# Kernel tuning notes

Measured on AMD Instinct MI355X. Metric: run time of the kernel, lower is better.

Reference implementation:

```python
import jax, jax.numpy as jnp
import numpy as np

T, U, H, P, UC = 256, 512, 64, 1024, 10000
LAMBDA_T = 0.1      # temporal decay rate (Flashback default scale)
LAMBDA_S = 100.0    # spatial decay rate
DAY = 86400.0


def setup_inputs() -> dict:
    key = jax.random.key(0)
    ks = jax.random.split(key, 12)
    sc = 0.02
    x = jax.random.randint(ks[0], (T, U), 0, P)
    # timestamps, increasing along the sequence axis (checkin order)
    t = jnp.sort(jax.random.uniform(ks[1], (T, U)) * (7.0 * DAY), axis=0)
    t_slot = jax.random.randint(ks[2], (T, U), 0, 168)
    s = jax.random.normal(ks[3], (T, U, 2))
    y = jax.random.randint(ks[4], (T, U), 0, P)
    h = jnp.zeros((U, H), jnp.float32)
    active_user = jax.random.randint(ks[5], (U,), 0, UC)
    poi_emb = jax.random.normal(ks[6], (P, H)) * sc
    user_emb = jax.random.normal(ks[7], (UC, H)) * sc
    Wx = jax.random.normal(ks[8], (H, 3 * H)) * sc
    Wh = jax.random.normal(ks[9], (H, 3 * H)) * sc
    b = jnp.zeros((3 * H,), jnp.float32)
    fc_W = jax.random.normal(ks[10], (2 * H, P)) * sc
    fc_b = jnp.zeros((P,), jnp.float32)
    return dict(x=x, t=t, t_slot=t_slot, s=s, y=y, h=h, active_user=active_user,
                poi_emb=poi_emb, user_emb=user_emb, Wx=Wx, Wh=Wh, b=b,
                fc_W=fc_W, fc_b=fc_b)


def _gru_scan(x_emb, h0, Wx, Wh, b):
    # x_emb: [T,U,H], h0: [U,H]
    def step(hprev, xt):
        gx = xt @ Wx + b          # [U,3H]
        gh = hprev @ Wh           # [U,3H]
        rx, zx, nx = jnp.split(gx, 3, axis=-1)
        rh, zh, nh = jnp.split(gh, 3, axis=-1)
        r = jax.nn.sigmoid(rx + rh)
        z = jax.nn.sigmoid(zx + zh)
        n = jnp.tanh(nx + r * nh)
        hn = (1.0 - z) * hprev + z * n
        return hn, hn
    hT, outs = jax.lax.scan(step, h0, x_emb)
    return outs, hT  # [T,U,H], [U,H]


def reference(x, t, t_slot, s, y, h, active_user,
              poi_emb, user_emb, Wx, Wh, b, fc_W, fc_b):
    seq_len, user_len = x.shape
    x_emb = poi_emb[x]                 # [T,U,H]  (stands in for pre_model emb)
    p_u = user_emb[active_user]        # [U,H]
    out, hT = _gru_scan(x_emb, h, Wx, Wh, b)  # RNN outputs [T,U,H]

    # Pairwise spatiotemporal decay weights, vectorized over (i,j,user).
    dt = t[:, None, :] - t[None, :, :]                    # [T,T,U]
    ds = jnp.linalg.norm(s[:, None, :, :] - s[None, :, :, :], axis=-1)  # [T,T,U]
    f_t = 0.5 * (jnp.cos(dt * (2.0 * jnp.pi / DAY)) + 1.0) * jnp.exp(-(dt / DAY) * LAMBDA_T)
    f_s = jnp.exp(-ds * LAMBDA_S)
    causal = jnp.tril(jnp.ones((seq_len, seq_len), dtype=bool))  # j <= i
    w = jnp.where(causal[:, :, None], f_t * f_s + 1e-10, 0.0)     # [T,T,U]
    sum_w = jnp.sum(w, axis=1)                                    # [T,U]
    out_w = jnp.einsum('iju,juh->iuh', w, out) / sum_w[:, :, None]  # [T,U,H]

    feats = jnp.concatenate(
        [out_w, jnp.broadcast_to(p_u[None], (seq_len, user_len, p_u.shape[-1]))],
        axis=-1)                                                  # [T,U,2H]
    y_linear = feats @ fc_W + fc_b                                # [T,U,P]
    return y_linear, hT
```

## Files before the change

### kernel.cpp

```cpp
#include <hip/hip_runtime.h>

#define T_N 256
#define U_N 512
#define H_N 64
#define P_N 1024

typedef __attribute__((ext_vector_type(8))) short short8;
typedef __attribute__((ext_vector_type(4))) short short4v;
typedef __attribute__((ext_vector_type(4))) float f32x4;

#define MFMA __builtin_amdgcn_mfma_f32_16x16x32_bf16

#define LGKM_BARRIER() asm volatile("s_waitcnt lgkmcnt(0)\ns_barrier" ::: "memory")

__device__ __forceinline__ short f2bf(float f) {
  union { float f; unsigned u; } v; v.f = f;
  unsigned r = v.u + 0x7FFFu + ((v.u >> 16) & 1u);
  return (short)(r >> 16);
}

__device__ __forceinline__ unsigned cvtpk(float lo, float hi) {
  unsigned r;
  asm("v_cvt_pk_bf16_f32 %0, %1, %2" : "=v"(r) : "v"(lo), "v"(hi));
  return r;
}

__device__ __forceinline__ short8 pack8(float4 a, float4 b) {
  union { unsigned u[4]; short8 s; } z;
  z.u[0] = cvtpk(a.x, a.y); z.u[1] = cvtpk(a.z, a.w);
  z.u[2] = cvtpk(b.x, b.y); z.u[3] = cvtpk(b.z, b.w);
  return z.s;
}

__device__ __forceinline__ float bfu_lo(unsigned u) {
  union { unsigned x; float f; } v; v.x = u << 16; return v.f;
}
__device__ __forceinline__ float bfu_hi(unsigned u) {
  union { unsigned x; float f; } v; v.x = u & 0xffff0000u; return v.f;
}

__global__ __launch_bounds__(256) void k_pack(
    const float* __restrict__ Wx, const float* __restrict__ Wh,
    const float* __restrict__ fcW, short* __restrict__ wxp,
    short* __restrict__ whp, short* __restrict__ bp) {
  if (blockIdx.x < 12) {
    int idx = blockIdx.x * 256 + threadIdx.x;
    int m = idx / 1536;
    int r = idx % 1536;
    const float* W = m ? Wh : Wx;
    short* op = m ? whp : wxp;
    int ks = r / 768, lk = (r / 192) & 3, g = r % 192;
#pragma unroll
    for (int e = 0; e < 8; ++e)
      op[(size_t)r * 8 + e] = f2bf(W[(ks * 32 + lk * 8 + e) * 192 + g]);
  } else {
    int sidx = (blockIdx.x - 12) * 256 + threadIdx.x;
    int s = sidx & 1023;
    int kg = (sidx >> 10) & 3;
    int ks = sidx >> 12;
    int L = (s & ~63) + 4 * (s & 15) + ((s >> 4) & 3);
#pragma unroll
    for (int e = 0; e < 8; ++e) {
      int k = ks * 32 + kg * 8 + e;
      bp[((size_t)((ks * 4 + kg) * P_N + s)) * 8 + e] = f2bf(fcW[k * P_N + L]);
    }
  }
}

__global__ __launch_bounds__(256) void k_gx(
    const int* __restrict__ x, const float* __restrict__ poi_emb,
    const short* __restrict__ wxp, const float* __restrict__ b,
    char* __restrict__ gxp) {
  int wave = threadIdx.x >> 6, lane = threadIdx.x & 63;
  int lr = lane & 15, lk = lane >> 4;
  int tile = blockIdx.x * 4 + wave;
  int row = tile * 16 + lr;
  int xv = x[row];
  const float* pb = poi_emb + (size_t)xv * H_N + lk * 8;
  float4 v0 = *(const float4*)pb, v1 = *(const float4*)(pb + 4);
  float4 v2 = *(const float4*)(pb + 32), v3 = *(const float4*)(pb + 36);
  short8 ax0 = pack8(v0, v1), ax1 = pack8(v2, v3);
#pragma unroll
  for (int j = 0; j < 12; ++j) {
    float bc = b[16 * j + lr];
    f32x4 acc = {bc, bc, bc, bc};
    short8 bf0 = *(const short8*)&wxp[((size_t)((0 * 4 + lk) * 192 + 16 * j + lr)) * 8];
    short8 bf1 = *(const short8*)&wxp[((size_t)((1 * 4 + lk) * 192 + 16 * j + lr)) * 8];
    acc = MFMA(ax0, bf0, acc, 0, 0, 0);
    acc = MFMA(ax1, bf1, acc, 0, 0, 0);
    uint2 pk;
    pk.x = cvtpk(acc[0], acc[1]);
    pk.y = cvtpk(acc[2], acc[3]);
    *(uint2*)(gxp + (((size_t)tile * 12 + j) * 64 + lane) * 8) = pk;
  }
}

__global__ __launch_bounds__(256) void k_scan2(
    const char* __restrict__ gxp, const float* __restrict__ h0,
    const short* __restrict__ whp, short* __restrict__ out_tr,
    float* __restrict__ hT) {
  int ublk = blockIdx.x;
  int u0 = ublk * 16;
  int tid = threadIdx.x;
  int w = tid >> 6, lane = tid & 63, lr = lane & 15, lk = lane >> 4;
  __shared__ __align__(16) float h_lds[8][16][68];
  int sgr = 16 * w, sgz = 64 + 16 * w, sgn = 128 + 16 * w;
  short8 fhr[2], fhz[2], fhn[2];
#pragma unroll
  for (int ks = 0; ks < 2; ++ks) {
    size_t base = (size_t)((ks * 4 + lk) * 192) * 8;
    fhr[ks] = *(const short8*)&whp[base + (size_t)(sgr + lr) * 8];
    fhz[ks] = *(const short8*)&whp[base + (size_t)(sgz + lr) * 8];
    fhn[ks] = *(const short8*)&whp[base + (size_t)(sgn + lr) * 8];
  }
  for (int idx = tid; idx < 16 * 64; idx += 256)
    h_lds[7][idx >> 6][idx & 63] = h0[(size_t)(u0 + (idx >> 6)) * H_N + (idx & 63)];
  __syncthreads();
  float hp[4];
#pragma unroll
  for (int e = 0; e < 4; ++e) hp[e] = h_lds[7][4 * lk + e][16 * w + lr];
  short8 ah0, ah1;
  {
    float4 q0 = *(float4*)&h_lds[7][lr][8 * lk];
    float4 q1 = *(float4*)&h_lds[7][lr][8 * lk + 4];
    float4 q2 = *(float4*)&h_lds[7][lr][32 + 8 * lk];
    float4 q3 = *(float4*)&h_lds[7][lr][32 + 8 * lk + 4];
    ah0 = pack8(q0, q1); ah1 = pack8(q2, q3);
  }
  const char* gbase = gxp + (((size_t)ublk * 12 + w) * 64 + lane) * 8;
  uint2 pr0, pr1, pr2, pr3, pz0, pz1, pz2, pz3, pn0, pn1, pn2, pn3;
#define PF(sl, tt) { size_t o = (size_t)(tt) * 196608; \
    pr##sl = *(const uint2*)(gbase + o); \
    pz##sl = *(const uint2*)(gbase + o + 2048); \
    pn##sl = *(const uint2*)(gbase + o + 4096); }
  PF(0, 0) PF(1, 1) PF(2, 2) PF(3, 3)
  for (int t8 = 0; t8 < T_N; t8 += 8) {
#define GATE(E, TB) { \
      float r = 1.f / (1.f + __expf(-accr[E])); \
      float z = 1.f / (1.f + __expf(-accz[E])); \
      float npre = accnx[E] + r * accnh[E]; \
      float e2 = __expf(2.f * npre); \
      float n = 1.f - 2.f / (e2 + 1.f); \
      float hn = hp[E] + z * (n - hp[E]); \
      hp[E] = hn; \
      h_lds[TB][4 * lk + E][16 * w + lr] = hn; }
#define BODY(TB, SL) { \
      f32x4 accr = {bfu_lo(pr##SL.x), bfu_hi(pr##SL.x), bfu_lo(pr##SL.y), bfu_hi(pr##SL.y)}; \
      f32x4 accz = {bfu_lo(pz##SL.x), bfu_hi(pz##SL.x), bfu_lo(pz##SL.y), bfu_hi(pz##SL.y)}; \
      f32x4 accnx = {bfu_lo(pn##SL.x), bfu_hi(pn##SL.x), bfu_lo(pn##SL.y), bfu_hi(pn##SL.y)}; \
      f32x4 accnh = {0.f, 0.f, 0.f, 0.f}; \
      int tpf = t8 + TB + 4; if (tpf > 255) tpf = 255; \
      PF(SL, tpf) \
      accr = MFMA(ah0, fhr[0], accr, 0, 0, 0); \
      accr = MFMA(ah1, fhr[1], accr, 0, 0, 0); \
      accz = MFMA(ah0, fhz[0], accz, 0, 0, 0); \
      accz = MFMA(ah1, fhz[1], accz, 0, 0, 0); \
      accnh = MFMA(ah0, fhn[0], accnh, 0, 0, 0); \
      accnh = MFMA(ah1, fhn[1], accnh, 0, 0, 0); \
      GATE(0, TB) GATE(1, TB) GATE(2, TB) GATE(3, TB) \
      LGKM_BARRIER(); \
      { \
        float4 q0 = *(float4*)&h_lds[TB][lr][8 * lk]; \
        float4 q1 = *(float4*)&h_lds[TB][lr][8 * lk + 4]; \
        float4 q2 = *(float4*)&h_lds[TB][lr][32 + 8 * lk]; \
        float4 q3 = *(float4*)&h_lds[TB][lr][32 + 8 * lk + 4]; \
        ah0 = pack8(q0, q1); ah1 = pack8(q2, q3); \
      } }
    BODY(0, 0) BODY(1, 1) BODY(2, 2) BODY(3, 3)
    BODY(4, 0) BODY(5, 1) BODY(6, 2) BODY(7, 3)
    {
      int tb = t8 >> 3;
#pragma unroll
      for (int pp = 0; pp < 4; ++pp) {
        int p = pp * 256 + tid;
        int uu = p >> 6, hh = p & 63;
        uint4 pkd;
        pkd.x = cvtpk(h_lds[0][uu][hh], h_lds[1][uu][hh]);
        pkd.y = cvtpk(h_lds[2][uu][hh], h_lds[3][uu][hh]);
        pkd.z = cvtpk(h_lds[4][uu][hh], h_lds[5][uu][hh]);
        pkd.w = cvtpk(h_lds[6][uu][hh], h_lds[7][uu][hh]);
        *(uint4*)&out_tr[((((size_t)(u0 + uu)) * 32 + tb) * 64 + hh) * 8] = pkd;
      }
    }
    LGKM_BARRIER();
  }
  for (int idx = tid; idx < 16 * 64; idx += 256)
    hT[(size_t)(u0 + (idx >> 6)) * H_N + (idx & 63)] = h_lds[7][idx >> 6][idx & 63];
}

__global__ __launch_bounds__(256) void k_ub(
    const int* __restrict__ active_user, const float* __restrict__ user_emb,
    const float* __restrict__ fcW, const float* __restrict__ fcb,
    float* __restrict__ ub) {
  int u = blockIdx.x;
  int tid = threadIdx.x;
  __shared__ float pu[H_N];
  if (tid < H_N) pu[tid] = user_emb[active_user[u] * H_N + tid];
  __syncthreads();
  for (int p = tid; p < P_N; p += 256) {
    float acc = fcb[p];
#pragma unroll
    for (int k = 0; k < H_N; ++k) acc += pu[k] * fcW[(H_N + k) * P_N + p];
    ub[u * P_N + p] = acc;
  }
}

__global__ __launch_bounds__(256, 4) void k_stage2(
    const float* __restrict__ t, const float* __restrict__ s,
    const short* __restrict__ out_tr, short* __restrict__ apk) {
  int u = blockIdx.x;
  int tid = threadIdx.x;
  __shared__ __align__(16) unsigned short wlT[16][264];
  __shared__ float tU[T_N];
  __shared__ float sUx[T_N], sUy[T_N];
  {
    int jr = tid;
    tU[jr] = t[jr * U_N + u];
    sUx[jr] = s[((size_t)jr * U_N + u) * 2];
    sUy[jr] = s[((size_t)jr * U_N + u) * 2 + 1];
  }
  __syncthreads();
  int lane = tid & 63, wv = tid >> 6;
  int lr = lane & 15, lk = lane >> 4;
  int j = tid;
  float tj = tU[j], sx = sUx[j], sy = sUy[j];
  const short* obase = out_tr + (size_t)u * 32 * 64 * 8;
  short8 ones;
#pragma unroll
  for (int e = 0; e < 8; ++e) ones[e] = (short)0x3F80;
  for (int c = 0; c < 16; ++c) {
#pragma unroll
    for (int iqq = 0; iqq < 16; ++iqq) {
      int i = c * 16 + iqq;
      float wv_ = 0.f;
      if (j <= i) {
        float dt = tU[i] - tj;
        float dx = sUx[i] - sx, dy = sUy[i] - sy;
        float dsn = sqrtf(dx * dx + dy * dy);
        float arg = dt * (-1.1574074074074074e-06f) - 100.0f * dsn;
        float ft = 0.5f * (__cosf(dt * 7.2722052166430395e-05f) + 1.0f);
        wv_ = ft * __expf(arg) + 1e-10f;
      }
      wlT[iqq][j] = (unsigned short)f2bf(wv_);
    }
    __syncthreads();
    f32x4 acc = {0.f, 0.f, 0.f, 0.f};
    f32x4 acc1 = {0.f, 0.f, 0.f, 0.f};
    int nk = (c + 2) >> 1;
    for (int kk = 0; kk < nk; ++kk) {
      short8 aw = *(const short8*)&wlT[lr][kk * 32 + 8 * lk];
      short8 bo = *(const short8*)&obase[(((kk * 4 + lk) * 64) + 16 * wv + lr) * 8];
      acc = MFMA(aw, bo, acc, 0, 0, 0);
      acc1 = MFMA(aw, ones, acc1, 0, 0, 0);
    }
#pragma unroll
    for (int e = 0; e < 4; ++e) {
      int i = c * 16 + 4 * lk + e;
      float val = acc[e] * (1.f / acc1[e]);
      apk[((size_t)i * U_N + u) * H_N + 16 * wv + lr] = f2bf(val);
    }
    __syncthreads();
  }
}

__global__ __launch_bounds__(256) void k_fc(
    const short* __restrict__ apk, const short* __restrict__ Bp,
    const float* __restrict__ ub, float* __restrict__ C) {
  int bm = blockIdx.y, bn = blockIdx.x;
  int tid = threadIdx.x;
  int wave = tid >> 6, lane = tid & 63;
  int wm = wave >> 1, wn = wave & 1;
  int row0 = bm * 128 + wm * 64;
  int col0 = bn * 128 + wn * 64;
  int lr = lane & 15, lk = lane >> 4;
  f32x4 acc[4][4] = {};
#pragma unroll
  for (int ks = 0; ks < 2; ++ks) {
    short8 af[4];
#pragma unroll
    for (int m = 0; m < 4; ++m)
      af[m] = *(const short8*)&apk[((size_t)(row0 + m * 16 + lr)) * H_N + ks * 32 + lk * 8];
#pragma unroll
    for (int n = 0; n < 4; ++n) {
      short8 bf = *(const short8*)&Bp[((size_t)((ks * 4 + lk) * P_N + col0 + n * 16 + lr)) * 8];
#pragma unroll
      for (int m = 0; m < 4; ++m)
        acc[m][n] = MFMA(af[m], bf, acc[m][n], 0, 0, 0);
    }
  }
#pragma unroll
  for (int m = 0; m < 4; ++m) {
    int rbase = row0 + m * 16 + lk * 4;
#pragma unroll
    for (int r = 0; r < 4; ++r) {
      int row = rbase + r;
      int uu = row & (U_N - 1);
      f32x4 ubv = *(const f32x4*)&ub[(size_t)uu * P_N + col0 + 4 * lr];
      f32x4 v;
      v[0] = acc[m][0][r] + ubv[0];
      v[1] = acc[m][1][r] + ubv[1];
      v[2] = acc[m][2][r] + ubv[2];
      v[3] = acc[m][3][r] + ubv[3];
      __builtin_nontemporal_store(v, (f32x4*)&C[(size_t)row * P_N + col0 + 4 * lr]);
    }
  }
}

extern "C" void kernel_launch(void* const* d_in, const int* in_sizes, int n_in,
                              void* d_out, int out_size, void* d_ws, size_t ws_size,
                              hipStream_t stream) {
  const int*   x           = (const int*)d_in[0];
  const float* t           = (const float*)d_in[1];
  const float* s           = (const float*)d_in[3];
  const float* h0          = (const float*)d_in[5];
  const int*   active_user = (const int*)d_in[6];
  const float* poi_emb     = (const float*)d_in[7];
  const float* user_emb    = (const float*)d_in[8];
  const float* Wx          = (const float*)d_in[9];
  const float* Wh          = (const float*)d_in[10];
  const float* b           = (const float*)d_in[11];
  const float* fcW         = (const float*)d_in[12];
  const float* fcb         = (const float*)d_in[13];

  float* y_out = (float*)d_out;
  float* hT = y_out + (size_t)T_N * U_N * P_N;

  char* ws = (char*)d_ws;
  short* out_tr = (short*)ws;
  char*  gxp    = ws + 16777216;
  short* apk    = (short*)(ws + 16777216);
  float* ub     = (float*)(ws + 67108864);
  short* bp     = (short*)(ws + 69206016);
  short* wxp    = (short*)(ws + 69337088);
  short* whp    = (short*)(ws + 69361664);

  k_pack<<<44, 256, 0, stream>>>(Wx, Wh, fcW, wxp, whp, bp);
  k_gx<<<2048, 256, 0, stream>>>(x, poi_emb, wxp, b, gxp);
  k_scan2<<<32, 256, 0, stream>>>(gxp, h0, whp, out_tr, hT);
  k_ub<<<U_N, 256, 0, stream>>>(active_user, user_emb, fcW, fcb, ub);
  k_stage2<<<U_N, 256, 0, stream>>>(t, s, out_tr, apk);
  k_fc<<<dim3(8, 1024), 256, 0, stream>>>(apk, bp, ub, y_out);
}
```

Baseline: 418.0 us.

## Factor decay weights via cos-difference identity, skip unused tiles, deepen GRU prefetch

```diff
diff --git a/kernel.cpp b/kernel.cpp
--- a/kernel.cpp
+++ b/kernel.cpp
@@ -128,12 +128,14 @@
     ah0 = pack8(q0, q1); ah1 = pack8(q2, q3);
   }
   const char* gbase = gxp + (((size_t)ublk * 12 + w) * 64 + lane) * 8;
-  uint2 pr0, pr1, pr2, pr3, pz0, pz1, pz2, pz3, pn0, pn1, pn2, pn3;
+  uint2 pr0, pr1, pr2, pr3, pr4, pr5, pr6, pr7;
+  uint2 pz0, pz1, pz2, pz3, pz4, pz5, pz6, pz7;
+  uint2 pn0, pn1, pn2, pn3, pn4, pn5, pn6, pn7;
 #define PF(sl, tt) { size_t o = (size_t)(tt) * 196608; \
     pr##sl = *(const uint2*)(gbase + o); \
     pz##sl = *(const uint2*)(gbase + o + 2048); \
     pn##sl = *(const uint2*)(gbase + o + 4096); }
-  PF(0, 0) PF(1, 1) PF(2, 2) PF(3, 3)
+  PF(0, 0) PF(1, 1) PF(2, 2) PF(3, 3) PF(4, 4) PF(5, 5) PF(6, 6) PF(7, 7)
   for (int t8 = 0; t8 < T_N; t8 += 8) {
 #define GATE(E, TB) { \
       float r = 1.f / (1.f + __expf(-accr[E])); \
@@ -149,7 +151,7 @@
       f32x4 accz = {bfu_lo(pz##SL.x), bfu_hi(pz##SL.x), bfu_lo(pz##SL.y), bfu_hi(pz##SL.y)}; \
       f32x4 accnx = {bfu_lo(pn##SL.x), bfu_hi(pn##SL.x), bfu_lo(pn##SL.y), bfu_hi(pn##SL.y)}; \
       f32x4 accnh = {0.f, 0.f, 0.f, 0.f}; \
-      int tpf = t8 + TB + 4; if (tpf > 255) tpf = 255; \
+      int tpf = t8 + TB + 8; if (tpf > 255) tpf = 255; \
       PF(SL, tpf) \
       accr = MFMA(ah0, fhr[0], accr, 0, 0, 0); \
       accr = MFMA(ah1, fhr[1], accr, 0, 0, 0); \
@@ -167,7 +169,7 @@
         ah0 = pack8(q0, q1); ah1 = pack8(q2, q3); \
       } }
     BODY(0, 0) BODY(1, 1) BODY(2, 2) BODY(3, 3)
-    BODY(4, 0) BODY(5, 1) BODY(6, 2) BODY(7, 3)
+    BODY(4, 4) BODY(5, 5) BODY(6, 6) BODY(7, 7)
     {
       int tb = t8 >> 3;
 #pragma unroll
@@ -211,42 +213,52 @@
   int u = blockIdx.x;
   int tid = threadIdx.x;
   __shared__ __align__(16) unsigned short wlT[16][264];
-  __shared__ float tU[T_N];
-  __shared__ float sUx[T_N], sUy[T_N];
+  __shared__ __align__(8) float csU[T_N][2];
+  __shared__ __align__(8) float seU[T_N][2];
+  __shared__ float eU[T_N];
+  float cj, sj, Fj, sx, sy;
   {
     int jr = tid;
-    tU[jr] = t[jr * U_N + u];
-    sUx[jr] = s[((size_t)jr * U_N + u) * 2];
-    sUy[jr] = s[((size_t)jr * U_N + u) * 2 + 1];
+    float tj = t[jr * U_N + u];
+    cj = __cosf(tj * 7.2722052166430395e-05f);
+    sj = __sinf(tj * 7.2722052166430395e-05f);
+    float ej = __expf(tj * -1.1574074074074074e-06f);
+    Fj = __expf(tj * 1.1574074074074074e-06f);
+    csU[jr][0] = cj; csU[jr][1] = sj;
+    eU[jr] = ej;
+    sx = s[((size_t)jr * U_N + u) * 2];
+    sy = s[((size_t)jr * U_N + u) * 2 + 1];
+    seU[jr][0] = sx; seU[jr][1] = sy;
   }
   __syncthreads();
   int lane = tid & 63, wv = tid >> 6;
   int lr = lane & 15, lk = lane >> 4;
   int j = tid;
-  float tj = tU[j], sx = sUx[j], sy = sUy[j];
   const short* obase = out_tr + (size_t)u * 32 * 64 * 8;
   short8 ones;
 #pragma unroll
   for (int e = 0; e < 8; ++e) ones[e] = (short)0x3F80;
   for (int c = 0; c < 16; ++c) {
-#pragma unroll
-    for (int iqq = 0; iqq < 16; ++iqq) {
-      int i = c * 16 + iqq;
-      float wv_ = 0.f;
-      if (j <= i) {
-        float dt = tU[i] - tj;
-        float dx = sUx[i] - sx, dy = sUy[i] - sy;
-        float dsn = sqrtf(dx * dx + dy * dy);
-        float arg = dt * (-1.1574074074074074e-06f) - 100.0f * dsn;
-        float ft = 0.5f * (__cosf(dt * 7.2722052166430395e-05f) + 1.0f);
-        wv_ = ft * __expf(arg) + 1e-10f;
+    int nk = (c + 2) >> 1;
+    if (wv * 64 < nk * 32) {
+#pragma unroll
+      for (int iqq = 0; iqq < 16; ++iqq) {
+        int i = c * 16 + iqq;
+        float ci = csU[i][0], si = csU[i][1];
+        float ei = eU[i];
+        float dx = seU[i][0] - sx, dy = seU[i][1] - sy;
+        float dsn = sqrtf(__builtin_fmaf(dx, dx, dy * dy));
+        float fs = __expf(-100.0f * dsn);
+        float ctm = __builtin_fmaf(ci, cj, si * sj);
+        float ft2 = __builtin_fmaf(0.5f, ctm, 0.5f);
+        float ww = __builtin_fmaf(ft2 * (ei * Fj), fs, 1e-10f);
+        ww = (j <= i) ? ww : 0.0f;
+        wlT[iqq][j] = (unsigned short)cvtpk(ww, ww);
       }
-      wlT[iqq][j] = (unsigned short)f2bf(wv_);
     }
     __syncthreads();
     f32x4 acc = {0.f, 0.f, 0.f, 0.f};
     f32x4 acc1 = {0.f, 0.f, 0.f, 0.f};
-    int nk = (c + 2) >> 1;
     for (int kk = 0; kk < nk; ++kk) {
       short8 aw = *(const short8*)&wlT[lr][kk * 32 + 8 * lk];
       short8 bo = *(const short8*)&obase[(((kk * 4 + lk) * 64) + 16 * wv + lr) * 8];
```

Result: faster. 391.0 us (-6.4%).
